# Kernel optimization log

Hardware: AMD Instinct MI355X
Metric: run time of the kernel (lower is better)

## Reference

```python
import jax, jax.numpy as jnp
import numpy as np
import math

DX = DZ = DATTN = DOUT = 1024
LX = LZ = 4096

def setup_inputs() -> dict:
    key = jax.random.key(0)
    ks = jax.random.split(key, 6)
    X = jax.random.normal(ks[0], (DX, LX), dtype=jnp.float32)
    Z = jax.random.normal(ks[1], (DZ, LZ), dtype=jnp.float32)
    mask = jax.random.randint(ks[2], (LZ, LX), 0, 2) > 0  # bool (lz, lx)
    Wq = jax.random.normal(ks[3], (DATTN, DX), dtype=jnp.float32) / math.sqrt(DATTN)
    bq = jnp.zeros((DATTN, 1), dtype=jnp.float32)
    Wk = jax.random.normal(ks[4], (DATTN, DZ), dtype=jnp.float32) / math.sqrt(DATTN)
    bk = jnp.zeros((DATTN, 1), dtype=jnp.float32)
    Wv = jax.random.normal(ks[5], (DOUT, DZ), dtype=jnp.float32) / math.sqrt(DOUT)
    bv = jnp.zeros((DOUT, 1), dtype=jnp.float32)
    return {"X": X, "Z": Z, "mask": mask, "Wq": Wq, "bq": bq,
            "Wk": Wk, "bk": bk, "Wv": Wv, "bv": bv}

def reference(X, Z, mask, Wq, bq, Wk, bk, Wv, bv):
    dattn_sqrt = math.sqrt(Wq.shape[0])
    q = Wq @ X + bq                      # (dattn, lx)
    k = Wk @ Z + bk                      # (dattn, lz)
    v = Wv @ Z + bv                      # (dout, lz)
    score = k.T @ q                      # (lz, lx)
    # masked_fill with -1000 happens BEFORE scaling, matching the original
    score = jnp.where(mask, score, jnp.float32(-1000.0))
    attn = jax.nn.softmax(score / dattn_sqrt, axis=0)  # softmax over lz (dim 0)
    return v @ attn                      # (dout, lx)
```

## Files before the change

kernel.cpp:

```cpp
#include <hip/hip_runtime.h>
#include <hip/hip_bf16.h>
#include <math.h>

constexpr int DXc = 1024;
constexpr int DZc = 1024;
constexpr int LXc = 4096;
constexpr int LZc = 4096;
constexpr int DAc = 1024;
constexpr int DOc = 1024;

typedef __attribute__((ext_vector_type(8))) short bf16x8;
typedef __attribute__((ext_vector_type(4))) float f32x4;

__device__ __forceinline__ ushort f2bf(float f) {
    __hip_bfloat16 h = __float2bfloat16(f);
    return *reinterpret_cast<ushort*>(&h);
}
__device__ __forceinline__ float bflo(unsigned u) {
    return __builtin_bit_cast(float, u << 16);
}
__device__ __forceinline__ float bfhi(unsigned u) {
    return __builtin_bit_cast(float, u & 0xffff0000u);
}

enum BiasMode { BIAS_NONE, BIAS_M, BIAS_N };

__device__ __forceinline__ void gemm_core(
    const ushort* __restrict__ A, const ushort* __restrict__ B,
    int K, int lda, int ldb, int m0, int n0, int kbase,
    ushort* As, ushort* Bs, f32x4 (*acc)[4])
{
    constexpr int BK = 32;
    const int tid = threadIdx.x;
    const int wv  = tid >> 6;
    const int wm  = (wv >> 1) * 64;
    const int wn  = (wv & 1) * 64;
    const int ln  = tid & 63;
    const int lrow = ln & 15;
    const int quad = ln >> 4;

    const int srow = tid >> 2;
    const int sseg = (tid & 3) * 8;
    const ushort* Ag = A + (size_t)(m0 + srow) * lda + sseg + kbase;
    const ushort* Bg = B + (size_t)(n0 + srow) * ldb + sseg + kbase;
    ushort* AsW = As + wv * 512;
    ushort* BsW = Bs + wv * 512;

    for (int k0 = 0; k0 < K; k0 += BK) {
        __syncthreads();
        __builtin_amdgcn_global_load_lds(
            (const __attribute__((address_space(1))) void*)(Ag + k0),
            (__attribute__((address_space(3))) void*)(AsW), 16, 0, 0);
        __builtin_amdgcn_global_load_lds(
            (const __attribute__((address_space(1))) void*)(Ag + (size_t)64 * lda + k0),
            (__attribute__((address_space(3))) void*)(AsW + 2048), 16, 0, 0);
        __builtin_amdgcn_global_load_lds(
            (const __attribute__((address_space(1))) void*)(Bg + k0),
            (__attribute__((address_space(3))) void*)(BsW), 16, 0, 0);
        __builtin_amdgcn_global_load_lds(
            (const __attribute__((address_space(1))) void*)(Bg + (size_t)64 * ldb + k0),
            (__attribute__((address_space(3))) void*)(BsW + 2048), 16, 0, 0);
        __syncthreads();

        bf16x8 af[4], bfr[4];
        #pragma unroll
        for (int t = 0; t < 4; ++t) {
            af[t]  = *reinterpret_cast<const bf16x8*>(&As[(wm + t * 16 + lrow) * BK + quad * 8]);
            bfr[t] = *reinterpret_cast<const bf16x8*>(&Bs[(wn + t * 16 + lrow) * BK + quad * 8]);
        }
        #pragma unroll
        for (int mi = 0; mi < 4; ++mi)
            #pragma unroll
            for (int nj = 0; nj < 4; ++nj)
                acc[mi][nj] = __builtin_amdgcn_mfma_f32_16x16x32_bf16(
                    af[mi], bfr[nj], acc[mi][nj], 0, 0, 0);
    }
}

template<BiasMode BMODE>
__device__ __forceinline__ void epi_bias_bf16(
    f32x4 (*acc)[4], const float* __restrict__ bias,
    ushort* __restrict__ C, int ldc, int m0, int n0)
{
    const int tid = threadIdx.x;
    const int wv  = tid >> 6;
    const int wm  = (wv >> 1) * 64;
    const int wn  = (wv & 1) * 64;
    const int lrow = tid & 15;
    const int quad = (tid & 63) >> 4;
    #pragma unroll
    for (int mi = 0; mi < 4; ++mi)
        #pragma unroll
        for (int r = 0; r < 4; ++r) {
            const int m = m0 + wm + mi * 16 + quad * 4 + r;
            const float bm = (BMODE == BIAS_M) ? bias[m] : 0.0f;
            #pragma unroll
            for (int nj = 0; nj < 4; ++nj) {
                const int n = n0 + wn + nj * 16 + lrow;
                const float v = acc[mi][nj][r] + ((BMODE == BIAS_N) ? bias[n] : bm);
                C[(size_t)m * ldc + n] = f2bf(v);
            }
        }
}

__global__ __launch_bounds__(256)
void proj_kernel(const ushort* __restrict__ XT, const ushort* __restrict__ ZT,
                 const ushort* __restrict__ Wqb, const ushort* __restrict__ Wkb,
                 const ushort* __restrict__ Wvb,
                 const float* __restrict__ bq, const float* __restrict__ bk,
                 const float* __restrict__ bv,
                 ushort* __restrict__ qT, ushort* __restrict__ kT,
                 ushort* __restrict__ vB)
{
    __shared__ __align__(16) ushort As[128 * 32];
    __shared__ __align__(16) ushort Bs[128 * 32];
    f32x4 acc[4][4] = {};
    int b = blockIdx.x;
    if (b < 256) {
        const int m0 = (b >> 3) * 128, n0 = (b & 7) * 128;
        gemm_core(XT, Wqb, DXc, DXc, DXc, m0, n0, 0, As, Bs, acc);
        epi_bias_bf16<BIAS_N>(acc, bq, qT, DAc, m0, n0);
    } else if (b < 512) {
        b -= 256;
        const int m0 = (b >> 3) * 128, n0 = (b & 7) * 128;
        gemm_core(ZT, Wkb, DZc, DZc, DZc, m0, n0, 0, As, Bs, acc);
        epi_bias_bf16<BIAS_N>(acc, bk, kT, DAc, m0, n0);
    } else {
        b -= 512;
        const int m0 = (b >> 5) * 128, n0 = (b & 31) * 128;
        gemm_core(Wvb, ZT, DZc, DZc, DZc, m0, n0, 0, As, Bs, acc);
        epi_bias_bf16<BIAS_M>(acc, bv, vB, LZc, m0, n0);
    }
}

__global__ __launch_bounds__(256)
void score_kernel(const ushort* __restrict__ qT, const ushort* __restrict__ kT,
                  ushort* __restrict__ sTb)
{
    __shared__ __align__(16) ushort As[128 * 32];
    __shared__ __align__(16) ushort Bs[128 * 32];
    f32x4 acc[4][4] = {};
    const int b = blockIdx.x;
    const int m0 = (b >> 5) * 128, n0 = (b & 31) * 128;
    gemm_core(qT, kT, DAc, DAc, DAc, m0, n0, 0, As, Bs, acc);
    epi_bias_bf16<BIAS_NONE>(acc, nullptr, sTb, LZc, m0, n0);
}

__global__ __launch_bounds__(256)
void expsum_kernel(ushort* __restrict__ sTb, const unsigned* __restrict__ bits,
                   float* __restrict__ rinv)
{
    const int x   = blockIdx.x;
    const int tid = threadIdx.x;
    ushort* row = sTb + (size_t)x * LZc;
    constexpr float scale = 1.0f / 32.0f;

    float sum = 0.0f;
    #pragma unroll
    for (int r = 0; r < 2; ++r) {
        uint4 pk = *reinterpret_cast<uint4*>(row + (size_t)(r * 256 + tid) * 8);
        unsigned* w = reinterpret_cast<unsigned*>(&pk);
        const unsigned mb = (bits[(size_t)x * 128 + r * 64 + (tid >> 2)] >> ((tid & 3) * 8)) & 0xffu;
        #pragma unroll
        for (int j = 0; j < 4; ++j) {
            const float lo = ((mb >> (2 * j))     & 1u) ? __expf(bflo(w[j]) * scale - 10.0f) : 0.0f;
            const float hi = ((mb >> (2 * j + 1)) & 1u) ? __expf(bfhi(w[j]) * scale - 10.0f) : 0.0f;
            const unsigned l = f2bf(lo), h = f2bf(hi);
            w[j] = l | (h << 16);
            sum += bflo(l) + bflo(h);
        }
        *reinterpret_cast<uint4*>(row + (size_t)(r * 256 + tid) * 8) = pk;
    }
    __shared__ float redsum[4];
    #pragma unroll
    for (int off = 32; off > 0; off >>= 1)
        sum += __shfl_down(sum, off, 64);
    if ((tid & 63) == 0) redsum[tid >> 6] = sum;
    __syncthreads();
    if (tid == 0) {
        const float s = redsum[0] + redsum[1] + redsum[2] + redsum[3];
        rinv[x] = 1.0f / fmaxf(s, 1e-35f);
    }
}

__global__ __launch_bounds__(256)
void out_kernel(const ushort* __restrict__ vB, const ushort* __restrict__ sTb,
                const float* __restrict__ rinv, float* __restrict__ out)
{
    __shared__ __align__(16) ushort As[128 * 32];
    __shared__ __align__(16) ushort Bs[128 * 32];
    f32x4 acc[4][4] = {};
    const int m0 = blockIdx.y * 128, n0 = blockIdx.x * 128;
    gemm_core(vB, sTb, LZc / 4, LZc, LZc, m0, n0, blockIdx.z * (LZc / 4), As, Bs, acc);

    const int tid = threadIdx.x;
    const int wv  = tid >> 6;
    const int wm  = (wv >> 1) * 64;
    const int wn  = (wv & 1) * 64;
    const int lrow = tid & 15;
    const int quad = (tid & 63) >> 4;

    float inv[4];
    int nn[4];
    #pragma unroll
    for (int nj = 0; nj < 4; ++nj) {
        nn[nj]  = n0 + wn + nj * 16 + lrow;
        inv[nj] = rinv[nn[nj]];
    }
    #pragma unroll
    for (int mi = 0; mi < 4; ++mi)
        #pragma unroll
        for (int r = 0; r < 4; ++r) {
            const int m = m0 + wm + mi * 16 + quad * 4 + r;
            #pragma unroll
            for (int nj = 0; nj < 4; ++nj)
                atomicAdd(&out[(size_t)m * LXc + nn[nj]], acc[mi][nj][r] * inv[nj]);
        }
}

__global__ __launch_bounds__(256)
void prep_kernel(const float* __restrict__ X, const float* __restrict__ Z,
                 const float* __restrict__ Wq, const float* __restrict__ Wk,
                 const float* __restrict__ Wv, const int* __restrict__ mask,
                 ushort* __restrict__ XT, ushort* __restrict__ ZT,
                 ushort* __restrict__ Wqb, ushort* __restrict__ Wkb,
                 ushort* __restrict__ Wvb, unsigned* __restrict__ bits)
{
    __shared__ float tile[32][33];
    const int tid = threadIdx.x;
    int b = blockIdx.x;

    if (b < 8192) {
        const float* in  = (b < 4096) ? X : Z;
        ushort*      out = (b < 4096) ? XT : ZT;
        const int local = b & 4095;
        const int c0 = (local & 127) * 32, r0 = (local >> 7) * 32;
        const int tx = tid & 31, ty = tid >> 5;
        #pragma unroll
        for (int i = 0; i < 32; i += 8)
            tile[ty + i][tx] = in[(size_t)(r0 + ty + i) * LXc + c0 + tx];
        __syncthreads();
        #pragma unroll
        for (int i = 0; i < 32; i += 8)
            out[(size_t)(c0 + ty + i) * DXc + r0 + tx] = f2bf(tile[tx][ty + i]);
        return;
    }
    if (b < 11264) {
        b -= 8192;
        const float* in  = (b < 1024) ? Wq : (b < 2048) ? Wk : Wv;
        ushort*      out = (b < 1024) ? Wqb : (b < 2048) ? Wkb : Wvb;
        const size_t i = ((size_t)(b & 1023) * 256 + tid) * 4;
        float4 f = *reinterpret_cast<const float4*>(in + i);
        ushort4 u;
        u.x = f2bf(f.x); u.y = f2bf(f.y); u.z = f2bf(f.z); u.w = f2bf(f.w);
        *reinterpret_cast<ushort4*>(out + i) = u;
        return;
    }
    b -= 11264;
    const int xb = b & 15, zb = b >> 4;
    const int x  = xb * 256 + tid;
    const int z0 = zb * 32;
    unsigned w = 0;
    #pragma unroll 8
    for (int i = 0; i < 32; ++i)
        w |= (mask[(size_t)(z0 + i) * LXc + x] != 0 ? 1u : 0u) << i;
    bits[(size_t)x * (LZc / 32) + zb] = w;
}

extern "C" void kernel_launch(void* const* d_in, const int* in_sizes, int n_in,
                              void* d_out, int out_size, void* d_ws, size_t ws_size,
                              hipStream_t stream)
{
    const float* X    = (const float*)d_in[0];
    const float* Z    = (const float*)d_in[1];
    const int*   mask = (const int*)  d_in[2];
    const float* Wq   = (const float*)d_in[3];
    const float* bq   = (const float*)d_in[4];
    const float* Wk   = (const float*)d_in[5];
    const float* bk   = (const float*)d_in[6];
    const float* Wv   = (const float*)d_in[7];
    const float* bv   = (const float*)d_in[8];
    float* out = (float*)d_out;

    char* ws = (char*)d_ws;
    ushort*   XT   = (ushort*)(ws);
    ushort*   ZT   = (ushort*)(ws + ( 8ull << 20));
    ushort*   Wqb  = (ushort*)(ws + (16ull << 20));
    ushort*   Wkb  = (ushort*)(ws + (18ull << 20));
    ushort*   Wvb  = (ushort*)(ws + (20ull << 20));
    ushort*   qT   = (ushort*)(ws + (22ull << 20));
    ushort*   kT   = (ushort*)(ws + (30ull << 20));
    ushort*   vB   = (ushort*)(ws + (38ull << 20));
    ushort*   sTb  = (ushort*)(ws + (46ull << 20));
    unsigned* bits = (unsigned*)(ws + (78ull << 20));
    float*    rinv = (float*)  (ws + (80ull << 20));

    hipMemsetAsync(out, 0, (size_t)DOc * LXc * sizeof(float), stream);
    prep_kernel<<<dim3(13312), 256, 0, stream>>>(X, Z, Wq, Wk, Wv, mask,
                                                 XT, ZT, Wqb, Wkb, Wvb, bits);
    proj_kernel<<<dim3(768), 256, 0, stream>>>(XT, ZT, Wqb, Wkb, Wvb,
                                               bq, bk, bv, qT, kT, vB);
    score_kernel<<<dim3(1024), 256, 0, stream>>>(qT, kT, sTb);
    expsum_kernel<<<dim3(LXc), 256, 0, stream>>>(sTb, bits, rinv);
    out_kernel<<<dim3(32, 8, 4), 256, 0, stream>>>(vB, sTb, rinv, out);
}
```

Before: 342.2 us.

## Fuse attention stages into one cooperative persistent kernel with grid syncs

Replaces the separate projection, score, exp-sum and output launches with a single cooperative kernel of 768 persistent blocks. Each stage walks its tiles in a grid-stride loop and the stages are separated by grid-wide barriers. The atomicAdd split-K epilogue becomes plain fp32 stores into four partial buffers, followed by a reduce phase that applies the softmax normalisation, so the output memset is no longer needed. This is meant to remove launch gaps and atomic contention. In exchange it adds 64MB of partial-buffer writes and reads, grid-barrier cost, and relies on 3 blocks per CU fitting for the cooperative launch, with a multi-kernel fallback if that launch fails.

Measured after the change: 736.3 us. 115% more time.

```diff
diff --git a/kernel.cpp b/kernel.cpp
--- a/kernel.cpp
+++ b/kernel.cpp
@@ -1,6 +1,9 @@
 #include <hip/hip_runtime.h>
 #include <hip/hip_bf16.h>
+#include <hip/hip_cooperative_groups.h>
 #include <math.h>
+
+namespace cg = cooperative_groups;
 
 constexpr int DXc = 1024;
 constexpr int DZc = 1024;
@@ -103,110 +106,15 @@
         }
 }
 
-__global__ __launch_bounds__(256)
-void proj_kernel(const ushort* __restrict__ XT, const ushort* __restrict__ ZT,
-                 const ushort* __restrict__ Wqb, const ushort* __restrict__ Wkb,
-                 const ushort* __restrict__ Wvb,
-                 const float* __restrict__ bq, const float* __restrict__ bk,
-                 const float* __restrict__ bv,
-                 ushort* __restrict__ qT, ushort* __restrict__ kT,
-                 ushort* __restrict__ vB)
-{
-    __shared__ __align__(16) ushort As[128 * 32];
-    __shared__ __align__(16) ushort Bs[128 * 32];
-    f32x4 acc[4][4] = {};
-    int b = blockIdx.x;
-    if (b < 256) {
-        const int m0 = (b >> 3) * 128, n0 = (b & 7) * 128;
-        gemm_core(XT, Wqb, DXc, DXc, DXc, m0, n0, 0, As, Bs, acc);
-        epi_bias_bf16<BIAS_N>(acc, bq, qT, DAc, m0, n0);
-    } else if (b < 512) {
-        b -= 256;
-        const int m0 = (b >> 3) * 128, n0 = (b & 7) * 128;
-        gemm_core(ZT, Wkb, DZc, DZc, DZc, m0, n0, 0, As, Bs, acc);
-        epi_bias_bf16<BIAS_N>(acc, bk, kT, DAc, m0, n0);
-    } else {
-        b -= 512;
-        const int m0 = (b >> 5) * 128, n0 = (b & 31) * 128;
-        gemm_core(Wvb, ZT, DZc, DZc, DZc, m0, n0, 0, As, Bs, acc);
-        epi_bias_bf16<BIAS_M>(acc, bv, vB, LZc, m0, n0);
-    }
-}
-
-__global__ __launch_bounds__(256)
-void score_kernel(const ushort* __restrict__ qT, const ushort* __restrict__ kT,
-                  ushort* __restrict__ sTb)
-{
-    __shared__ __align__(16) ushort As[128 * 32];
-    __shared__ __align__(16) ushort Bs[128 * 32];
-    f32x4 acc[4][4] = {};
-    const int b = blockIdx.x;
-    const int m0 = (b >> 5) * 128, n0 = (b & 31) * 128;
-    gemm_core(qT, kT, DAc, DAc, DAc, m0, n0, 0, As, Bs, acc);
-    epi_bias_bf16<BIAS_NONE>(acc, nullptr, sTb, LZc, m0, n0);
-}
-
-__global__ __launch_bounds__(256)
-void expsum_kernel(ushort* __restrict__ sTb, const unsigned* __restrict__ bits,
-                   float* __restrict__ rinv)
-{
-    const int x   = blockIdx.x;
-    const int tid = threadIdx.x;
-    ushort* row = sTb + (size_t)x * LZc;
-    constexpr float scale = 1.0f / 32.0f;
-
-    float sum = 0.0f;
-    #pragma unroll
-    for (int r = 0; r < 2; ++r) {
-        uint4 pk = *reinterpret_cast<uint4*>(row + (size_t)(r * 256 + tid) * 8);
-        unsigned* w = reinterpret_cast<unsigned*>(&pk);
-        const unsigned mb = (bits[(size_t)x * 128 + r * 64 + (tid >> 2)] >> ((tid & 3) * 8)) & 0xffu;
-        #pragma unroll
-        for (int j = 0; j < 4; ++j) {
-            const float lo = ((mb >> (2 * j))     & 1u) ? __expf(bflo(w[j]) * scale - 10.0f) : 0.0f;
-            const float hi = ((mb >> (2 * j + 1)) & 1u) ? __expf(bfhi(w[j]) * scale - 10.0f) : 0.0f;
-            const unsigned l = f2bf(lo), h = f2bf(hi);
-            w[j] = l | (h << 16);
-            sum += bflo(l) + bflo(h);
-        }
-        *reinterpret_cast<uint4*>(row + (size_t)(r * 256 + tid) * 8) = pk;
-    }
-    __shared__ float redsum[4];
-    #pragma unroll
-    for (int off = 32; off > 0; off >>= 1)
-        sum += __shfl_down(sum, off, 64);
-    if ((tid & 63) == 0) redsum[tid >> 6] = sum;
-    __syncthreads();
-    if (tid == 0) {
-        const float s = redsum[0] + redsum[1] + redsum[2] + redsum[3];
-        rinv[x] = 1.0f / fmaxf(s, 1e-35f);
-    }
-}
-
-__global__ __launch_bounds__(256)
-void out_kernel(const ushort* __restrict__ vB, const ushort* __restrict__ sTb,
-                const float* __restrict__ rinv, float* __restrict__ out)
-{
-    __shared__ __align__(16) ushort As[128 * 32];
-    __shared__ __align__(16) ushort Bs[128 * 32];
-    f32x4 acc[4][4] = {};
-    const int m0 = blockIdx.y * 128, n0 = blockIdx.x * 128;
-    gemm_core(vB, sTb, LZc / 4, LZc, LZc, m0, n0, blockIdx.z * (LZc / 4), As, Bs, acc);
-
+__device__ __forceinline__ void epi_f32(
+    f32x4 (*acc)[4], float* __restrict__ C, int ldc, int m0, int n0)
+{
     const int tid = threadIdx.x;
     const int wv  = tid >> 6;
     const int wm  = (wv >> 1) * 64;
     const int wn  = (wv & 1) * 64;
     const int lrow = tid & 15;
     const int quad = (tid & 63) >> 4;
-
-    float inv[4];
-    int nn[4];
-    #pragma unroll
-    for (int nj = 0; nj < 4; ++nj) {
-        nn[nj]  = n0 + wn + nj * 16 + lrow;
-        inv[nj] = rinv[nn[nj]];
-    }
     #pragma unroll
     for (int mi = 0; mi < 4; ++mi)
         #pragma unroll
@@ -214,8 +122,172 @@
             const int m = m0 + wm + mi * 16 + quad * 4 + r;
             #pragma unroll
             for (int nj = 0; nj < 4; ++nj)
-                atomicAdd(&out[(size_t)m * LXc + nn[nj]], acc[mi][nj][r] * inv[nj]);
-        }
+                C[(size_t)m * ldc + (n0 + wn + nj * 16 + lrow)] = acc[mi][nj][r];
+        }
+}
+
+__device__ __forceinline__ void phase_proj(
+    const ushort* XT, const ushort* ZT, const ushort* Wqb, const ushort* Wkb,
+    const ushort* Wvb, const float* bq, const float* bk, const float* bv,
+    ushort* qT, ushort* kT, ushort* vB, ushort* As, ushort* Bs)
+{
+    for (int b = blockIdx.x; b < 768; b += gridDim.x) {
+        f32x4 acc[4][4] = {};
+        if (b < 256) {
+            const int m0 = (b >> 3) * 128, n0 = (b & 7) * 128;
+            gemm_core(XT, Wqb, DXc, DXc, DXc, m0, n0, 0, As, Bs, acc);
+            epi_bias_bf16<BIAS_N>(acc, bq, qT, DAc, m0, n0);
+        } else if (b < 512) {
+            const int bb = b - 256;
+            const int m0 = (bb >> 3) * 128, n0 = (bb & 7) * 128;
+            gemm_core(ZT, Wkb, DZc, DZc, DZc, m0, n0, 0, As, Bs, acc);
+            epi_bias_bf16<BIAS_N>(acc, bk, kT, DAc, m0, n0);
+        } else {
+            const int bb = b - 512;
+            const int m0 = (bb >> 5) * 128, n0 = (bb & 31) * 128;
+            gemm_core(Wvb, ZT, DZc, DZc, DZc, m0, n0, 0, As, Bs, acc);
+            epi_bias_bf16<BIAS_M>(acc, bv, vB, LZc, m0, n0);
+        }
+    }
+}
+
+__device__ __forceinline__ void phase_score(
+    const ushort* qT, const ushort* kT, ushort* sTb, ushort* As, ushort* Bs)
+{
+    for (int b = blockIdx.x; b < 1024; b += gridDim.x) {
+        f32x4 acc[4][4] = {};
+        const int m0 = (b >> 5) * 128, n0 = (b & 31) * 128;
+        gemm_core(qT, kT, DAc, DAc, DAc, m0, n0, 0, As, Bs, acc);
+        epi_bias_bf16<BIAS_NONE>(acc, nullptr, sTb, LZc, m0, n0);
+    }
+}
+
+__device__ __forceinline__ void phase_expsum(
+    ushort* sTb, const unsigned* bits, float* rinv)
+{
+    __shared__ float redsum[4];
+    const int tid = threadIdx.x;
+    for (int x = blockIdx.x; x < LXc; x += gridDim.x) {
+        ushort* row = sTb + (size_t)x * LZc;
+        constexpr float scale = 1.0f / 32.0f;
+        float sum = 0.0f;
+        #pragma unroll
+        for (int r = 0; r < 2; ++r) {
+            uint4 pk = *reinterpret_cast<uint4*>(row + (size_t)(r * 256 + tid) * 8);
+            unsigned* w = reinterpret_cast<unsigned*>(&pk);
+            const unsigned mb = (bits[(size_t)x * 128 + r * 64 + (tid >> 2)] >> ((tid & 3) * 8)) & 0xffu;
+            #pragma unroll
+            for (int j = 0; j < 4; ++j) {
+                const float lo = ((mb >> (2 * j))     & 1u) ? __expf(bflo(w[j]) * scale - 10.0f) : 0.0f;
+                const float hi = ((mb >> (2 * j + 1)) & 1u) ? __expf(bfhi(w[j]) * scale - 10.0f) : 0.0f;
+                const unsigned l = f2bf(lo), h = f2bf(hi);
+                w[j] = l | (h << 16);
+                sum += bflo(l) + bflo(h);
+            }
+            *reinterpret_cast<uint4*>(row + (size_t)(r * 256 + tid) * 8) = pk;
+        }
+        #pragma unroll
+        for (int off = 32; off > 0; off >>= 1)
+            sum += __shfl_down(sum, off, 64);
+        if ((tid & 63) == 0) redsum[tid >> 6] = sum;
+        __syncthreads();
+        if (tid == 0) {
+            const float s = redsum[0] + redsum[1] + redsum[2] + redsum[3];
+            rinv[x] = 1.0f / fmaxf(s, 1e-35f);
+        }
+        __syncthreads();
+    }
+}
+
+__device__ __forceinline__ void phase_out(
+    const ushort* vB, const ushort* sTb, float* P, ushort* As, ushort* Bs)
+{
+    for (int b = blockIdx.x; b < 1024; b += gridDim.x) {
+        f32x4 acc[4][4] = {};
+        const int zs = b >> 8, rem = b & 255;
+        const int m0 = (rem >> 5) * 128, n0 = (rem & 31) * 128;
+        gemm_core(vB, sTb, LZc / 4, LZc, LZc, m0, n0, zs * (LZc / 4), As, Bs, acc);
+        epi_f32(acc, P + (size_t)zs * DOc * LXc, LXc, m0, n0);
+    }
+}
+
+__device__ __forceinline__ void phase_reduce(
+    const float* P, const float* rinv, float* out)
+{
+    constexpr size_t total = (size_t)DOc * LXc;
+    const int tid = threadIdx.x;
+    for (int b = blockIdx.x; b < 4096; b += gridDim.x) {
+        const size_t i = (size_t)b * 1024 + tid * 4;
+        float4 s = *reinterpret_cast<const float4*>(P + i);
+        #pragma unroll
+        for (int p = 1; p < 4; ++p) {
+            const float4 t = *reinterpret_cast<const float4*>(P + (size_t)p * total + i);
+            s.x += t.x; s.y += t.y; s.z += t.z; s.w += t.w;
+        }
+        const float4 l = *reinterpret_cast<const float4*>(rinv + (i & (LXc - 1)));
+        s.x *= l.x; s.y *= l.y; s.z *= l.z; s.w *= l.w;
+        *reinterpret_cast<float4*>(out + i) = s;
+    }
+}
+
+__global__ __launch_bounds__(256, 3)
+void fused_kernel(const ushort* __restrict__ XT, const ushort* __restrict__ ZT,
+                  const ushort* __restrict__ Wqb, const ushort* __restrict__ Wkb,
+                  const ushort* __restrict__ Wvb,
+                  const float* __restrict__ bq, const float* __restrict__ bk,
+                  const float* __restrict__ bv,
+                  ushort* __restrict__ qT, ushort* __restrict__ kT,
+                  ushort* __restrict__ vB, ushort* __restrict__ sTb,
+                  const unsigned* __restrict__ bits, float* __restrict__ rinv,
+                  float* __restrict__ P, float* __restrict__ out)
+{
+    __shared__ __align__(16) ushort As[128 * 32];
+    __shared__ __align__(16) ushort Bs[128 * 32];
+    cg::grid_group grid = cg::this_grid();
+
+    phase_proj(XT, ZT, Wqb, Wkb, Wvb, bq, bk, bv, qT, kT, vB, As, Bs);
+    grid.sync();
+    phase_score(qT, kT, sTb, As, Bs);
+    grid.sync();
+    phase_expsum(sTb, bits, rinv);
+    grid.sync();
+    phase_out(vB, sTb, P, As, Bs);
+    grid.sync();
+    phase_reduce(P, rinv, out);
+}
+
+__global__ __launch_bounds__(256)
+void proj_k(const ushort* XT, const ushort* ZT, const ushort* Wqb,
+            const ushort* Wkb, const ushort* Wvb, const float* bq,
+            const float* bk, const float* bv, ushort* qT, ushort* kT, ushort* vB)
+{
+    __shared__ __align__(16) ushort As[128 * 32];
+    __shared__ __align__(16) ushort Bs[128 * 32];
+    phase_proj(XT, ZT, Wqb, Wkb, Wvb, bq, bk, bv, qT, kT, vB, As, Bs);
+}
+__global__ __launch_bounds__(256)
+void score_k(const ushort* qT, const ushort* kT, ushort* sTb)
+{
+    __shared__ __align__(16) ushort As[128 * 32];
+    __shared__ __align__(16) ushort Bs[128 * 32];
+    phase_score(qT, kT, sTb, As, Bs);
+}
+__global__ __launch_bounds__(256)
+void expsum_k(ushort* sTb, const unsigned* bits, float* rinv)
+{
+    phase_expsum(sTb, bits, rinv);
+}
+__global__ __launch_bounds__(256)
+void out_k(const ushort* vB, const ushort* sTb, float* P)
+{
+    __shared__ __align__(16) ushort As[128 * 32];
+    __shared__ __align__(16) ushort Bs[128 * 32];
+    phase_out(vB, sTb, P, As, Bs);
+}
+__global__ __launch_bounds__(256)
+void reduce_k(const float* P, const float* rinv, float* out)
+{
+    phase_reduce(P, rinv, out);
 }
 
 __global__ __launch_bounds__(256)
@@ -290,17 +362,28 @@
     ushort*   Wvb  = (ushort*)(ws + (20ull << 20));
     ushort*   qT   = (ushort*)(ws + (22ull << 20));
     ushort*   kT   = (ushort*)(ws + (30ull << 20));
-    ushort*   vB   = (ushort*)(ws + (38ull << 20));
-    ushort*   sTb  = (ushort*)(ws + (46ull << 20));
-    unsigned* bits = (unsigned*)(ws + (78ull << 20));
-    float*    rinv = (float*)  (ws + (80ull << 20));
-
-    hipMemsetAsync(out, 0, (size_t)DOc * LXc * sizeof(float), stream);
+    float*    P    = (float*) (ws);
+    ushort*   vB   = (ushort*)(ws + (64ull << 20));
+    ushort*   sTb  = (ushort*)(ws + (72ull << 20));
+    unsigned* bits = (unsigned*)(ws + (104ull << 20));
+    float*    rinv = (float*)  (ws + (106ull << 20));
+
     prep_kernel<<<dim3(13312), 256, 0, stream>>>(X, Z, Wq, Wk, Wv, mask,
                                                  XT, ZT, Wqb, Wkb, Wvb, bits);
-    proj_kernel<<<dim3(768), 256, 0, stream>>>(XT, ZT, Wqb, Wkb, Wvb,
-                                               bq, bk, bv, qT, kT, vB);
-    score_kernel<<<dim3(1024), 256, 0, stream>>>(qT, kT, sTb);
-    expsum_kernel<<<dim3(LXc), 256, 0, stream>>>(sTb, bits, rinv);
-    out_kernel<<<dim3(32, 8, 4), 256, 0, stream>>>(vB, sTb, rinv, out);
-}
+
+    void* args[] = { (void*)&XT, (void*)&ZT, (void*)&Wqb, (void*)&Wkb, (void*)&Wvb,
+                     (void*)&bq, (void*)&bk, (void*)&bv,
+                     (void*)&qT, (void*)&kT, (void*)&vB, (void*)&sTb,
+                     (void*)&bits, (void*)&rinv, (void*)&P, (void*)&out };
+    hipError_t err = hipLaunchCooperativeKernel((void*)fused_kernel, dim3(768),
+                                                dim3(256), args, 0, stream);
+    if (err != hipSuccess) {
+        (void)hipGetLastError();
+        proj_k<<<dim3(768), 256, 0, stream>>>(XT, ZT, Wqb, Wkb, Wvb,
+                                              bq, bk, bv, qT, kT, vB);
+        score_k<<<dim3(1024), 256, 0, stream>>>(qT, kT, sTb);
+        expsum_k<<<dim3(4096), 256, 0, stream>>>(sTb, bits, rinv);
+        out_k<<<dim3(1024), 256, 0, stream>>>(vB, sTb, P);
+        reduce_k<<<dim3(4096), 256, 0, stream>>>(P, rinv, out);
+    }
+}
```
